# Kernel tuning notes

Hardware: AMD Instinct MI355X
Metric: run time of the kernel (lower is better)

## Reference

```python
import jax, jax.numpy as jnp
import numpy as np

PARTITIONS = [1, 2, 4, 8, 16, 32]
FORECAST = 720
D_MODEL = 256
B, C = 64, 64


def len_of_split_into_k_parts(L, k):
    avg, rem = L // k, L % k
    return [avg + (1 if i < rem else 0) for i in range(k)]


def setup_inputs() -> dict:
    key = jax.random.key(0)
    keys = jax.random.split(key, 1 + 2 * len(PARTITIONS))
    T = sum(PARTITIONS)
    inp = {"x": jax.random.normal(keys[0], (B, C, T, D_MODEL), dtype=jnp.float32)}
    for i, k in enumerate(PARTITIONS):
        max_len = max(len_of_split_into_k_parts(FORECAST, k))
        bound = 1.0 / np.sqrt(D_MODEL)
        inp[f"W{i}"] = jax.random.uniform(keys[1 + 2 * i], (max_len, D_MODEL), minval=-bound, maxval=bound, dtype=jnp.float32)
        inp[f"b{i}"] = jax.random.uniform(keys[2 + 2 * i], (max_len,), minval=-bound, maxval=bound, dtype=jnp.float32)
    return inp


def _forward(x, Ws, bs):
    idx = 0
    total = None
    for i, k in enumerate(PARTITIONS):
        split = len_of_split_into_k_parts(FORECAST, k)
        x_r = x[..., idx:idx + k, :]                      # [B, C, k, d]
        idx += k
        proj = jnp.einsum('bctd,md->bctm', x_r, Ws[i]) + bs[i]  # [B, C, k, max_len]
        # ragged slice+concat: token s contributes its first split[s] positions
        tok = np.repeat(np.arange(k), split)              # [f] static indices
        pos = np.concatenate([np.arange(s) for s in split])  # [f]
        res = proj[..., tok, pos]                         # [B, C, f]
        total = res if total is None else total + res
    return jnp.swapaxes(total, -1, -2)                    # [B, f, C]


def reference(x, W0, b0, W1, b1, W2, b2, W3, b3, W4, b4, W5, b5):
    Ws = [W0, W1, W2, W3, W4, W5]
    bs = [b0, b1, b2, b3, b4, b5]
    return _forward(x, Ws, bs)
```

## Files before the change

kernel.cpp:

```cpp
#include <hip/hip_runtime.h>
#include <stdint.h>


#define FDIM 720
#define DDIM 256
#define TDIM 63
#define NSUBTOT 299
#define TAB_BYTES ((size_t)NSUBTOT * 8 * 1024)
#define OUTELEMS ((size_t)64 * FDIM * 64)
#define NPREPTHR (NSUBTOT * 8 * 64)

typedef __attribute__((ext_vector_type(8))) short short8;
typedef __attribute__((ext_vector_type(4))) float f32x4;

__device__ __forceinline__ uint32_t pkru(float a, float b) {
    uint32_t ua = __builtin_bit_cast(uint32_t, a) + 0x8000u;
    uint32_t ub = __builtin_bit_cast(uint32_t, b) + 0x8000u;
    return __builtin_amdgcn_perm(ub, ua, 0x07060302u);
}
__device__ __forceinline__ short8 loadpack(const float* p) {
    float4 v0 = *(const float4*)p;
    float4 v1 = *(const float4*)(p + 4);
    uint4 u;
    u.x = pkru(v0.x, v0.y);
    u.y = pkru(v0.z, v0.w);
    u.z = pkru(v1.x, v1.y);
    u.w = pkru(v1.z, v1.w);
    return __builtin_bit_cast(short8, u);
}

__device__ __forceinline__ void atomAddF(float* p, float v) {
    unsafeAtomicAdd(p, v);
}

__device__ __forceinline__ void jpos(int i, int f, int& j, int& pos) {
    switch (i) {
        case 0: j = 0;       pos = f;            break;
        case 1: j = f / 360; pos = f - 360 * j;  break;
        case 2: j = f / 180; pos = f - 180 * j;  break;
        case 3: j = f / 90;  pos = f - 90 * j;   break;
        case 4: j = f / 45;  pos = f - 45 * j;   break;
        default:
            if (f < 368) { j = f / 23;  pos = f - 23 * j; }
            else { int g = f - 368; int q = g / 22; j = 16 + q; pos = g - 22 * q; }
            break;
    }
}

__device__ __forceinline__ void tok_params(int tok, int& len, int& ns,
                                           int& start, int& tabsub) {
    if (tok < 1)       { len = 720; ns = 45; start = 0;
                         tabsub = 0; }
    else if (tok < 3)  { int j = tok - 1;  len = 360; ns = 23; start = 360 * j;
                         tabsub = 45 + j * 23; }
    else if (tok < 7)  { int j = tok - 3;  len = 180; ns = 12; start = 180 * j;
                         tabsub = 91 + j * 12; }
    else if (tok < 15) { int j = tok - 7;  len = 90;  ns = 6;  start = 90 * j;
                         tabsub = 139 + j * 6; }
    else if (tok < 31) { int j = tok - 15; len = 45;  ns = 3;  start = 45 * j;
                         tabsub = 187 + j * 3; }
    else               { int j = tok - 31;
                         len = (j < 16) ? 23 : 22;
                         start = (j < 16) ? 23 * j : 368 + 22 * (j - 16);
                         ns = 2; tabsub = 235 + j * 2; }
}

__global__ __launch_bounds__(256) void olrs_prepinit(
    const float* __restrict__ W0, const float* __restrict__ W1,
    const float* __restrict__ W2, const float* __restrict__ W3,
    const float* __restrict__ W4, const float* __restrict__ W5,
    const float* __restrict__ b0, const float* __restrict__ b1,
    const float* __restrict__ b2, const float* __restrict__ b3,
    const float* __restrict__ b4, const float* __restrict__ b5,
    char* __restrict__ ws, float* __restrict__ out)
{
    const int gid = blockIdx.x * 256 + threadIdx.x;

    const size_t base = (size_t)gid * 4;
    if (base < OUTELEMS) {
        const int f = (int)((base >> 6) % FDIM);
        int j, p;
        float s = b0[f];
        jpos(1, f, j, p); s += b1[p];
        jpos(2, f, j, p); s += b2[p];
        jpos(3, f, j, p); s += b3[p];
        jpos(4, f, j, p); s += b4[p];
        jpos(5, f, j, p); s += b5[p];
        float4 o = {s, s, s, s};
        *(float4*)(out + base) = o;
    }

    if (gid < NPREPTHR) {
        const int lane = gid & 63;
        const int fid  = gid >> 6;
        const int ks = fid & 7;
        const int g  = fid >> 3;

        int len; const float* W; int s;
        if (g < 45)       { W = W0; len = 720; s = g; }
        else if (g < 91)  { int g2 = g - 45;  W = W1; len = 360; s = g2 % 23; }
        else if (g < 139) { int g2 = g - 91;  W = W2; len = 180; s = g2 % 12; }
        else if (g < 187) { int g2 = g - 139; W = W3; len = 90;  s = g2 % 6; }
        else if (g < 235) { int g2 = g - 187; W = W4; len = 45;  s = g2 % 3; }
        else              { int g2 = g - 235; W = W5; int j = g2 >> 1;
                            len = (j < 16) ? 23 : 22; s = g2 & 1; }

        const int m15  = lane & 15;
        const int koct = lane >> 4;
        const int pos  = s * 16 + m15;
        uint4 u = {0u, 0u, 0u, 0u};
        if (pos < len) {
            const float* src = W + (size_t)pos * DDIM + ks * 32 + koct * 8;
            float4 v0 = *(const float4*)src;
            float4 v1 = *(const float4*)(src + 4);
            u.x = pkru(v0.x, v0.y);
            u.y = pkru(v0.z, v0.w);
            u.z = pkru(v1.x, v1.y);
            u.w = pkru(v1.z, v1.w);
        }
        *(uint4*)(ws + (size_t)fid * 1024 + lane * 16) = u;
    }
}

__global__ __launch_bounds__(256) void olrs_main8(
    const float* __restrict__ x,
    const char* __restrict__ ws,
    float* __restrict__ out)
{
    __shared__ char lds[32768];

    const int bid   = blockIdx.x;
    const int rid   = bid >> 7;
    const int ntile = bid & 127;
    const int w     = threadIdx.x >> 6;
    const int lane  = threadIdx.x & 63;
    const int b     = ntile >> 1;
    const int c0    = (ntile & 1) << 5;
    const int m15   = lane & 15;
    const int koct  = lane >> 4;

    int tok, s0, slab;
    bool shx;
    if (rid < 2)      { tok = 0;            s0 = rid * 24 + w * 6; shx = true;  slab = 0; }
    else if (rid < 4) { tok = rid - 1;      s0 = w * 6;            shx = true;  slab = 0; }
    else if (rid < 6) { int tb = 3 + (rid - 4) * 2;
                        tok = tb + (w >> 1); s0 = (w & 1) * 6;     shx = true;  slab = w >> 1; }
    else              { tok = 7 + (rid - 6) * 4 + w; s0 = 0;       shx = false; slab = 0; }

    int len, ns, start, tabsub;
    tok_params(tok, len, ns, start, tabsub);
    const int send = (s0 + 6 < ns) ? (s0 + 6) : ns;

    short8 xl[8], xh[8];
    if (shx) {
        const int nslab   = (rid >= 4 && rid < 6) ? 2 : 1;
        const int tokbase = (rid < 2) ? 0 : ((rid < 4) ? (rid - 1) : 3 + (rid - 4) * 2);
        const int cc = threadIdx.x >> 3;
        const int t8 = threadIdx.x & 7;
        for (int sl = 0; sl < nslab; sl++) {
            const float* src = x + (((size_t)(b * 64 + c0 + cc)) * TDIM + tokbase + sl) * DDIM;
            char* dst = lds + sl * 16384;
            #pragma unroll
            for (int rep = 0; rep < 4; rep++) {
                const int d8 = t8 + rep * 8;
                float4 v0 = *(const float4*)(src + d8 * 8);
                float4 v1 = *(const float4*)(src + d8 * 8 + 4);
                uint4 u;
                u.x = pkru(v0.x, v0.y);
                u.y = pkru(v0.z, v0.w);
                u.z = pkru(v1.x, v1.y);
                u.w = pkru(v1.z, v1.w);
                const int slot = ((d8 >> 2) * 2 + (cc >> 4)) * 64
                               + (d8 & 3) * 16 + (cc & 15);
                *(uint4*)(dst + slot * 16) = u;
            }
        }
        __syncthreads();
        const char* sb = lds + slab * 16384;
        #pragma unroll
        for (int ks = 0; ks < 8; ks++) {
            xl[ks] = *(const short8*)(sb + ((ks * 2 + 0) * 64 + lane) * 16);
            xh[ks] = *(const short8*)(sb + ((ks * 2 + 1) * 64 + lane) * 16);
        }
    } else {
        const float* xpl = x + (((size_t)(b * 64 + c0 + m15)) * TDIM + tok) * DDIM;
        const float* xph = xpl + (size_t)16 * TDIM * DDIM;
        #pragma unroll
        for (int ks = 0; ks < 8; ks++)
            xl[ks] = loadpack(xpl + ks * 32 + koct * 8);
        #pragma unroll
        for (int ks = 0; ks < 8; ks++)
            xh[ks] = loadpack(xph + ks * 32 + koct * 8);
    }

    const char* tab = ws + (size_t)tabsub * 8192 + lane * 16;
    float* obl = out + ((size_t)b * FDIM + start) * 64 + c0 + m15;
    float* obh = obl + 16;

    short8 wA[8], wB[8];

    auto loadW = [&](short8* wreg, int s) {
        const char* t = tab + (size_t)s * 8192;
        #pragma unroll
        for (int ks = 0; ks < 8; ks++)
            wreg[ks] = *(const short8*)(t + ks * 1024);
    };
    auto compute = [&](const short8* wreg, int s) {
        f32x4 al0 = {0.f, 0.f, 0.f, 0.f}, al1 = {0.f, 0.f, 0.f, 0.f};
        f32x4 ah0 = {0.f, 0.f, 0.f, 0.f}, ah1 = {0.f, 0.f, 0.f, 0.f};
        __builtin_amdgcn_s_setprio(1);
        #pragma unroll
        for (int ks = 0; ks < 8; ks += 2) {
            al0 = __builtin_amdgcn_mfma_f32_16x16x32_bf16(wreg[ks],     xl[ks],     al0, 0, 0, 0);
            ah0 = __builtin_amdgcn_mfma_f32_16x16x32_bf16(wreg[ks],     xh[ks],     ah0, 0, 0, 0);
            al1 = __builtin_amdgcn_mfma_f32_16x16x32_bf16(wreg[ks + 1], xl[ks + 1], al1, 0, 0, 0);
            ah1 = __builtin_amdgcn_mfma_f32_16x16x32_bf16(wreg[ks + 1], xh[ks + 1], ah1, 0, 0, 0);
        }
        __builtin_amdgcn_s_setprio(0);
        const int fl0 = s * 16 + koct * 4;
        #pragma unroll
        for (int rg = 0; rg < 4; rg++) {
            const int fl = fl0 + rg;
            if (fl < len) {
                atomAddF(obl + (size_t)fl * 64, al0[rg] + al1[rg]);
                atomAddF(obh + (size_t)fl * 64, ah0[rg] + ah1[rg]);
            }
        }
    };

    int s = s0;
    loadW(wA, s);
    for (;;) {
        if (s + 1 < send) loadW(wB, s + 1);
        compute(wA, s);
        if (++s >= send) break;
        if (s + 1 < send) loadW(wA, s + 1);
        compute(wB, s);
        if (++s >= send) break;
    }
}

__device__ __forceinline__ int startf(int i, int j) {
    switch (i) {
        case 0: return 0;
        case 1: return 360 * j;
        case 2: return 180 * j;
        case 3: return 90 * j;
        case 4: return 45 * j;
        default: return (j < 16) ? 23 * j : 368 + 22 * (j - 16);
    }
}

__global__ __launch_bounds__(256) void olrs_fb(
    const float* __restrict__ x,
    const float* __restrict__ W0, const float* __restrict__ b0,
    const float* __restrict__ W1, const float* __restrict__ b1,
    const float* __restrict__ W2, const float* __restrict__ b2,
    const float* __restrict__ W3, const float* __restrict__ b3,
    const float* __restrict__ W4, const float* __restrict__ b4,
    const float* __restrict__ W5, const float* __restrict__ b5,
    float* __restrict__ out)
{
    const float* Wp[6] = {W0, W1, W2, W3, W4, W5};
    const float* bp[6] = {b0, b1, b2, b3, b4, b5};
    const int TB[6] = {0, 1, 3, 7, 15, 31};

    const int wid  = blockIdx.x * 4 + (threadIdx.x >> 6);
    const int lane = threadIdx.x & 63;
    const int ft   = wid % 45;
    const int bc   = wid / 45;
    const int b    = bc >> 2;
    const int c0   = (bc & 3) << 4;
    const int f0   = ft << 4;
    const int m15  = lane & 15;
    const int koct = lane >> 4;
    const size_t xrow = (size_t)(b * 64 + c0 + m15) * TDIM;

    f32x4 acc = {0.f, 0.f, 0.f, 0.f};
    #pragma unroll
    for (int i = 0; i < 6; i++) {
        int jlo, plo, jhi, phi;
        jpos(i, f0, jlo, plo);
        jpos(i, f0 + 15, jhi, phi);
        const bool cross = (jhi > jlo);
        const int fb = cross ? (startf(i, jhi) - f0) : 16;
        const float* xlo = x + (xrow + TB[i] + jlo) * DDIM;
        const float* xhi = x + (xrow + TB[i] + jhi) * DDIM;
        int jw, pw;
        jpos(i, f0 + m15, jw, pw);
        const float* wsrc = Wp[i] + (size_t)pw * DDIM;
        #pragma unroll
        for (int ks = 0; ks < 8; ks++) {
            const int d0 = ks * 32 + koct * 8;
            short8 a = loadpack(wsrc + d0);
            short8 blo = loadpack(xlo + d0);
            if (!cross) {
                acc = __builtin_amdgcn_mfma_f32_16x16x32_bf16(a, blo, acc, 0, 0, 0);
            } else {
                short8 bhi = loadpack(xhi + d0);
                short8 z;
                #pragma unroll
                for (int q = 0; q < 8; q++) z[q] = 0;
                short8 alo = (m15 < fb) ? a : z;
                short8 ahi = (m15 < fb) ? z : a;
                acc = __builtin_amdgcn_mfma_f32_16x16x32_bf16(alo, blo, acc, 0, 0, 0);
                acc = __builtin_amdgcn_mfma_f32_16x16x32_bf16(ahi, bhi, acc, 0, 0, 0);
            }
        }
    }
    #pragma unroll
    for (int rg = 0; rg < 4; rg++) {
        const int f = f0 + koct * 4 + rg;
        float bias = 0.f;
        #pragma unroll
        for (int i = 0; i < 6; i++) {
            int j, pos;
            jpos(i, f, j, pos);
            bias += bp[i][pos];
        }
        out[((size_t)b * FDIM + f) * 64 + c0 + m15] = acc[rg] + bias;
    }
}

extern "C" void kernel_launch(void* const* d_in, const int* in_sizes, int n_in,
                              void* d_out, int out_size, void* d_ws, size_t ws_size,
                              hipStream_t stream) {
    (void)in_sizes; (void)n_in; (void)out_size;

    const float* x  = (const float*)d_in[0];
    const float* W0 = (const float*)d_in[1];
    const float* b0 = (const float*)d_in[2];
    const float* W1 = (const float*)d_in[3];
    const float* b1 = (const float*)d_in[4];
    const float* W2 = (const float*)d_in[5];
    const float* b2 = (const float*)d_in[6];
    const float* W3 = (const float*)d_in[7];
    const float* b3 = (const float*)d_in[8];
    const float* W4 = (const float*)d_in[9];
    const float* b4 = (const float*)d_in[10];
    const float* W5 = (const float*)d_in[11];
    const float* b5 = (const float*)d_in[12];
    float* out = (float*)d_out;

    if (ws_size >= TAB_BYTES) {
        char* ws = (char*)d_ws;
        olrs_prepinit<<<dim3((unsigned)(OUTELEMS / 4 / 256)), dim3(256), 0, stream>>>(
            W0, W1, W2, W3, W4, W5, b0, b1, b2, b3, b4, b5, ws, out);
        olrs_main8<<<dim3(20 * 128), dim3(256), 0, stream>>>(x, ws, out);
    } else {
        olrs_fb<<<dim3(45 * 256), dim3(256), 0, stream>>>(
            x, W0, b0, W1, b1, W2, b2, W3, b3, W4, b4, W5, b5, out);
    }
}
```

Measured before the change: 86.60 us.

## Halve channel tile per block and drop weight double-buffering

Each block now covers 16 channels instead of 32, which doubles the grid to 5120 blocks and halves both the LDS footprint and the per-thread x registers. The explicit register double-buffering of weight tiles is removed, so weights are loaded inline right before each MFMA pair. The aim is lower register and LDS pressure, giving higher occupancy and more parallelism. The cost is that each weight tile is now fetched twice as often across blocks (once per 16-channel tile), and load latency is no longer hidden by the manual prefetch.

New measurement: 101.7 us. +17.4%, slower.

```diff
diff --git a/kernel.cpp b/kernel.cpp
--- a/kernel.cpp
+++ b/kernel.cpp
@@ -28,7 +28,6 @@
     u.w = pkru(v1.z, v1.w);
     return __builtin_bit_cast(short8, u);
 }
-
 __device__ __forceinline__ void atomAddF(float* p, float v) {
     unsafeAtomicAdd(p, v);
 }
@@ -122,47 +121,47 @@
     }
 }
 
-__global__ __launch_bounds__(256) void olrs_main8(
+__global__ __launch_bounds__(256) void olrs_main13(
     const float* __restrict__ x,
     const char* __restrict__ ws,
     float* __restrict__ out)
 {
-    __shared__ char lds[32768];
+    __shared__ char lds[16384];
 
     const int bid   = blockIdx.x;
-    const int rid   = bid >> 7;
-    const int ntile = bid & 127;
+    const int rid   = bid >> 8;
+    const int ntile = bid & 255;
     const int w     = threadIdx.x >> 6;
     const int lane  = threadIdx.x & 63;
-    const int b     = ntile >> 1;
-    const int c0    = (ntile & 1) << 5;
+    const int b     = ntile >> 2;
+    const int c0    = (ntile & 3) << 4;
     const int m15   = lane & 15;
     const int koct  = lane >> 4;
 
     int tok, s0, slab;
     bool shx;
-    if (rid < 2)      { tok = 0;            s0 = rid * 24 + w * 6; shx = true;  slab = 0; }
-    else if (rid < 4) { tok = rid - 1;      s0 = w * 6;            shx = true;  slab = 0; }
+    if (rid < 2)      { tok = 0;             s0 = rid * 24 + w * 6; shx = true;  slab = 0; }
+    else if (rid < 4) { tok = rid - 1;       s0 = w * 6;            shx = true;  slab = 0; }
     else if (rid < 6) { int tb = 3 + (rid - 4) * 2;
-                        tok = tb + (w >> 1); s0 = (w & 1) * 6;     shx = true;  slab = w >> 1; }
-    else              { tok = 7 + (rid - 6) * 4 + w; s0 = 0;       shx = false; slab = 0; }
+                        tok = tb + (w >> 1); s0 = (w & 1) * 6;      shx = true;  slab = w >> 1; }
+    else              { tok = 7 + (rid - 6) * 4 + w; s0 = 0;        shx = false; slab = 0; }
 
     int len, ns, start, tabsub;
     tok_params(tok, len, ns, start, tabsub);
     const int send = (s0 + 6 < ns) ? (s0 + 6) : ns;
 
-    short8 xl[8], xh[8];
+    short8 xf[8];
     if (shx) {
         const int nslab   = (rid >= 4 && rid < 6) ? 2 : 1;
         const int tokbase = (rid < 2) ? 0 : ((rid < 4) ? (rid - 1) : 3 + (rid - 4) * 2);
-        const int cc = threadIdx.x >> 3;
-        const int t8 = threadIdx.x & 7;
+        const int cc  = threadIdx.x >> 4;
+        const int t16 = threadIdx.x & 15;
         for (int sl = 0; sl < nslab; sl++) {
             const float* src = x + (((size_t)(b * 64 + c0 + cc)) * TDIM + tokbase + sl) * DDIM;
-            char* dst = lds + sl * 16384;
+            char* dst = lds + sl * 8192;
             #pragma unroll
-            for (int rep = 0; rep < 4; rep++) {
-                const int d8 = t8 + rep * 8;
+            for (int rep = 0; rep < 2; rep++) {
+                const int d8 = t16 + rep * 16;
                 float4 v0 = *(const float4*)(src + d8 * 8);
                 float4 v1 = *(const float4*)(src + d8 * 8 + 4);
                 uint4 u;
@@ -170,73 +169,44 @@
                 u.y = pkru(v0.z, v0.w);
                 u.z = pkru(v1.x, v1.y);
                 u.w = pkru(v1.z, v1.w);
-                const int slot = ((d8 >> 2) * 2 + (cc >> 4)) * 64
-                               + (d8 & 3) * 16 + (cc & 15);
+                const int slot = (d8 >> 2) * 64 + (d8 & 3) * 16 + cc;
                 *(uint4*)(dst + slot * 16) = u;
             }
         }
         __syncthreads();
-        const char* sb = lds + slab * 16384;
-        #pragma unroll
-        for (int ks = 0; ks < 8; ks++) {
-            xl[ks] = *(const short8*)(sb + ((ks * 2 + 0) * 64 + lane) * 16);
-            xh[ks] = *(const short8*)(sb + ((ks * 2 + 1) * 64 + lane) * 16);
-        }
+        const char* sb = lds + slab * 8192;
+        #pragma unroll
+        for (int ks = 0; ks < 8; ks++)
+            xf[ks] = *(const short8*)(sb + (ks * 64 + lane) * 16);
     } else {
-        const float* xpl = x + (((size_t)(b * 64 + c0 + m15)) * TDIM + tok) * DDIM;
-        const float* xph = xpl + (size_t)16 * TDIM * DDIM;
+        const float* xp = x + (((size_t)(b * 64 + c0 + m15)) * TDIM + tok) * DDIM;
         #pragma unroll
         for (int ks = 0; ks < 8; ks++)
-            xl[ks] = loadpack(xpl + ks * 32 + koct * 8);
-        #pragma unroll
-        for (int ks = 0; ks < 8; ks++)
-            xh[ks] = loadpack(xph + ks * 32 + koct * 8);
+            xf[ks] = loadpack(xp + ks * 32 + koct * 8);
     }
 
     const char* tab = ws + (size_t)tabsub * 8192 + lane * 16;
-    float* obl = out + ((size_t)b * FDIM + start) * 64 + c0 + m15;
-    float* obh = obl + 16;
-
-    short8 wA[8], wB[8];
-
-    auto loadW = [&](short8* wreg, int s) {
-        const char* t = tab + (size_t)s * 8192;
-        #pragma unroll
-        for (int ks = 0; ks < 8; ks++)
-            wreg[ks] = *(const short8*)(t + ks * 1024);
-    };
-    auto compute = [&](const short8* wreg, int s) {
-        f32x4 al0 = {0.f, 0.f, 0.f, 0.f}, al1 = {0.f, 0.f, 0.f, 0.f};
-        f32x4 ah0 = {0.f, 0.f, 0.f, 0.f}, ah1 = {0.f, 0.f, 0.f, 0.f};
+    float* obase = out + ((size_t)b * FDIM + start) * 64 + c0 + m15;
+
+    for (int s = s0; s < send; s++) {
+        f32x4 a0 = {0.f, 0.f, 0.f, 0.f};
+        f32x4 a1 = {0.f, 0.f, 0.f, 0.f};
+        const char* tsub = tab + (size_t)s * 8192;
         __builtin_amdgcn_s_setprio(1);
         #pragma unroll
         for (int ks = 0; ks < 8; ks += 2) {
-            al0 = __builtin_amdgcn_mfma_f32_16x16x32_bf16(wreg[ks],     xl[ks],     al0, 0, 0, 0);
-            ah0 = __builtin_amdgcn_mfma_f32_16x16x32_bf16(wreg[ks],     xh[ks],     ah0, 0, 0, 0);
-            al1 = __builtin_amdgcn_mfma_f32_16x16x32_bf16(wreg[ks + 1], xl[ks + 1], al1, 0, 0, 0);
-            ah1 = __builtin_amdgcn_mfma_f32_16x16x32_bf16(wreg[ks + 1], xh[ks + 1], ah1, 0, 0, 0);
+            short8 w0 = *(const short8*)(tsub + ks * 1024);
+            short8 w1 = *(const short8*)(tsub + (ks + 1) * 1024);
+            a0 = __builtin_amdgcn_mfma_f32_16x16x32_bf16(w0, xf[ks],     a0, 0, 0, 0);
+            a1 = __builtin_amdgcn_mfma_f32_16x16x32_bf16(w1, xf[ks + 1], a1, 0, 0, 0);
         }
         __builtin_amdgcn_s_setprio(0);
         const int fl0 = s * 16 + koct * 4;
         #pragma unroll
         for (int rg = 0; rg < 4; rg++) {
             const int fl = fl0 + rg;
-            if (fl < len) {
-                atomAddF(obl + (size_t)fl * 64, al0[rg] + al1[rg]);
-                atomAddF(obh + (size_t)fl * 64, ah0[rg] + ah1[rg]);
-            }
-        }
-    };
-
-    int s = s0;
-    loadW(wA, s);
-    for (;;) {
-        if (s + 1 < send) loadW(wB, s + 1);
-        compute(wA, s);
-        if (++s >= send) break;
-        if (s + 1 < send) loadW(wA, s + 1);
-        compute(wB, s);
-        if (++s >= send) break;
+            if (fl < len) atomAddF(obase + (size_t)fl * 64, a0[rg] + a1[rg]);
+        }
     }
 }
 
@@ -346,7 +316,7 @@
         char* ws = (char*)d_ws;
         olrs_prepinit<<<dim3((unsigned)(OUTELEMS / 4 / 256)), dim3(256), 0, stream>>>(
             W0, W1, W2, W3, W4, W5, b0, b1, b2, b3, b4, b5, ws, out);
-        olrs_main8<<<dim3(20 * 128), dim3(256), 0, stream>>>(x, ws, out);
+        olrs_main13<<<dim3(20 * 256), dim3(256), 0, stream>>>(x, ws, out);
     } else {
         olrs_fb<<<dim3(45 * 256), dim3(256), 0, stream>>>(
             x, W0, b0, W1, b1, W2, b2, W3, b3, W4, b4, W5, b5, out);
```

## Share weight tiles via LDS across waves for small-token partitions

Applied to the files above, without the earlier changes.

Blocks for the later partitions (tokens 7 and up) are remapped: each block now stages that token's bf16 weight sub-tiles into LDS once, and its four waves each handle a different (batch, channel) tile while reading weights from shared memory. Previously every wave fetched its own weights from global memory. The token-8 group is also split into two halves of three sub-tiles for more parallelism. The grid grows from 2560 to 2816 blocks and adds a barrier plus LDS staging per block, in exchange for less redundant global weight traffic.

New measurement: 92.44 us. 6.7% more time.

```diff
diff --git a/kernel.cpp b/kernel.cpp
--- a/kernel.cpp
+++ b/kernel.cpp
@@ -122,7 +122,7 @@
     }
 }
 
-__global__ __launch_bounds__(256) void olrs_main8(
+__global__ __launch_bounds__(256) void olrs_main15(
     const float* __restrict__ x,
     const char* __restrict__ ws,
     float* __restrict__ out)
@@ -130,30 +130,28 @@
     __shared__ char lds[32768];
 
     const int bid   = blockIdx.x;
-    const int rid   = bid >> 7;
-    const int ntile = bid & 127;
     const int w     = threadIdx.x >> 6;
     const int lane  = threadIdx.x & 63;
-    const int b     = ntile >> 1;
-    const int c0    = (ntile & 1) << 5;
     const int m15   = lane & 15;
     const int koct  = lane >> 4;
 
-    int tok, s0, slab;
-    bool shx;
-    if (rid < 2)      { tok = 0;            s0 = rid * 24 + w * 6; shx = true;  slab = 0; }
-    else if (rid < 4) { tok = rid - 1;      s0 = w * 6;            shx = true;  slab = 0; }
-    else if (rid < 6) { int tb = 3 + (rid - 4) * 2;
-                        tok = tb + (w >> 1); s0 = (w & 1) * 6;     shx = true;  slab = w >> 1; }
-    else              { tok = 7 + (rid - 6) * 4 + w; s0 = 0;       shx = false; slab = 0; }
-
-    int len, ns, start, tabsub;
-    tok_params(tok, len, ns, start, tabsub);
-    const int send = (s0 + 6 < ns) ? (s0 + 6) : ns;
-
-    short8 xl[8], xh[8];
-    if (shx) {
-        const int nslab   = (rid >= 4 && rid < 6) ? 2 : 1;
+    if (bid < 768) {
+        const int rid   = bid >> 7;
+        const int ntile = bid & 127;
+        const int b     = ntile >> 1;
+        const int c0    = (ntile & 1) << 5;
+
+        int tok, s0, slab;
+        if (rid < 2)      { tok = 0;             s0 = rid * 24 + w * 6; slab = 0; }
+        else if (rid < 4) { tok = rid - 1;       s0 = w * 6;            slab = 0; }
+        else              { int tb = 3 + (rid - 4) * 2;
+                            tok = tb + (w >> 1); s0 = (w & 1) * 6;      slab = w >> 1; }
+
+        int len, ns, start, tabsub;
+        tok_params(tok, len, ns, start, tabsub);
+        const int send = (s0 + 6 < ns) ? (s0 + 6) : ns;
+
+        const int nslab   = (rid >= 4) ? 2 : 1;
         const int tokbase = (rid < 2) ? 0 : ((rid < 4) ? (rid - 1) : 3 + (rid - 4) * 2);
         const int cc = threadIdx.x >> 3;
         const int t8 = threadIdx.x & 7;
@@ -176,67 +174,126 @@
             }
         }
         __syncthreads();
+        short8 xl[8], xh[8];
         const char* sb = lds + slab * 16384;
         #pragma unroll
         for (int ks = 0; ks < 8; ks++) {
             xl[ks] = *(const short8*)(sb + ((ks * 2 + 0) * 64 + lane) * 16);
             xh[ks] = *(const short8*)(sb + ((ks * 2 + 1) * 64 + lane) * 16);
         }
+
+        const char* tab = ws + (size_t)tabsub * 8192 + lane * 16;
+        float* obl = out + ((size_t)b * FDIM + start) * 64 + c0 + m15;
+        float* obh = obl + 16;
+
+        short8 wA[8], wB[8];
+        auto loadW = [&](short8* wreg, int s) {
+            const char* t = tab + (size_t)s * 8192;
+            #pragma unroll
+            for (int ks = 0; ks < 8; ks++)
+                wreg[ks] = *(const short8*)(t + ks * 1024);
+        };
+        auto compute = [&](const short8* wreg, int s) {
+            f32x4 al0 = {0.f, 0.f, 0.f, 0.f}, al1 = {0.f, 0.f, 0.f, 0.f};
+            f32x4 ah0 = {0.f, 0.f, 0.f, 0.f}, ah1 = {0.f, 0.f, 0.f, 0.f};
+            __builtin_amdgcn_s_setprio(1);
+            #pragma unroll
+            for (int ks = 0; ks < 8; ks += 2) {
+                al0 = __builtin_amdgcn_mfma_f32_16x16x32_bf16(wreg[ks],     xl[ks],     al0, 0, 0, 0);
+                ah0 = __builtin_amdgcn_mfma_f32_16x16x32_bf16(wreg[ks],     xh[ks],     ah0, 0, 0, 0);
+                al1 = __builtin_amdgcn_mfma_f32_16x16x32_bf16(wreg[ks + 1], xl[ks + 1], al1, 0, 0, 0);
+                ah1 = __builtin_amdgcn_mfma_f32_16x16x32_bf16(wreg[ks + 1], xh[ks + 1], ah1, 0, 0, 0);
+            }
+            __builtin_amdgcn_s_setprio(0);
+            const int fl0 = s * 16 + koct * 4;
+            #pragma unroll
+            for (int rg = 0; rg < 4; rg++) {
+                const int fl = fl0 + rg;
+                if (fl < len) {
+                    atomAddF(obl + (size_t)fl * 64, al0[rg] + al1[rg]);
+                    atomAddF(obh + (size_t)fl * 64, ah0[rg] + ah1[rg]);
+                }
+            }
+        };
+
+        int s = s0;
+        loadW(wA, s);
+        for (;;) {
+            if (s + 1 < send) loadW(wB, s + 1);
+            compute(wA, s);
+            if (++s >= send) break;
+            if (s + 1 < send) loadW(wA, s + 1);
+            compute(wB, s);
+            if (++s >= send) break;
+        }
     } else {
+        const int idx = bid - 768;
+        int tok, s0g, g;
+        if (idx < 512)       { int q = idx >> 5; g = idx & 31;
+                               tok = 7 + (q >> 1); s0g = (q & 1) * 3; }
+        else if (idx < 1024) { int q = idx - 512; g = q & 31;
+                               tok = 15 + (q >> 5); s0g = 0; }
+        else                 { int q = idx - 1024; g = q & 31;
+                               tok = 31 + (q >> 5); s0g = 0; }
+
+        int len, ns, start, tabsub;
+        tok_params(tok, len, ns, start, tabsub);
+        const int send = (s0g + 3 < ns) ? (s0g + 3) : ns;
+        const int nsub = send - s0g;
+
+        const int ntile = g * 4 + w;
+        const int b     = ntile >> 1;
+        const int c0    = (ntile & 1) << 5;
+
+        {
+            const char* src = ws + (size_t)(tabsub + s0g) * 8192;
+            const int nrep = nsub * 2;
+            for (int r = 0; r < nrep; r++) {
+                const int off = threadIdx.x * 16 + r * 4096;
+                *(uint4*)(lds + off) = *(const uint4*)(src + off);
+            }
+        }
+
         const float* xpl = x + (((size_t)(b * 64 + c0 + m15)) * TDIM + tok) * DDIM;
         const float* xph = xpl + (size_t)16 * TDIM * DDIM;
+        short8 xl[8], xh[8];
         #pragma unroll
         for (int ks = 0; ks < 8; ks++)
             xl[ks] = loadpack(xpl + ks * 32 + koct * 8);
         #pragma unroll
         for (int ks = 0; ks < 8; ks++)
             xh[ks] = loadpack(xph + ks * 32 + koct * 8);
-    }
-
-    const char* tab = ws + (size_t)tabsub * 8192 + lane * 16;
-    float* obl = out + ((size_t)b * FDIM + start) * 64 + c0 + m15;
-    float* obh = obl + 16;
-
-    short8 wA[8], wB[8];
-
-    auto loadW = [&](short8* wreg, int s) {
-        const char* t = tab + (size_t)s * 8192;
-        #pragma unroll
-        for (int ks = 0; ks < 8; ks++)
-            wreg[ks] = *(const short8*)(t + ks * 1024);
-    };
-    auto compute = [&](const short8* wreg, int s) {
-        f32x4 al0 = {0.f, 0.f, 0.f, 0.f}, al1 = {0.f, 0.f, 0.f, 0.f};
-        f32x4 ah0 = {0.f, 0.f, 0.f, 0.f}, ah1 = {0.f, 0.f, 0.f, 0.f};
-        __builtin_amdgcn_s_setprio(1);
-        #pragma unroll
-        for (int ks = 0; ks < 8; ks += 2) {
-            al0 = __builtin_amdgcn_mfma_f32_16x16x32_bf16(wreg[ks],     xl[ks],     al0, 0, 0, 0);
-            ah0 = __builtin_amdgcn_mfma_f32_16x16x32_bf16(wreg[ks],     xh[ks],     ah0, 0, 0, 0);
-            al1 = __builtin_amdgcn_mfma_f32_16x16x32_bf16(wreg[ks + 1], xl[ks + 1], al1, 0, 0, 0);
-            ah1 = __builtin_amdgcn_mfma_f32_16x16x32_bf16(wreg[ks + 1], xh[ks + 1], ah1, 0, 0, 0);
-        }
-        __builtin_amdgcn_s_setprio(0);
-        const int fl0 = s * 16 + koct * 4;
-        #pragma unroll
-        for (int rg = 0; rg < 4; rg++) {
-            const int fl = fl0 + rg;
-            if (fl < len) {
-                atomAddF(obl + (size_t)fl * 64, al0[rg] + al1[rg]);
-                atomAddF(obh + (size_t)fl * 64, ah0[rg] + ah1[rg]);
-            }
-        }
-    };
-
-    int s = s0;
-    loadW(wA, s);
-    for (;;) {
-        if (s + 1 < send) loadW(wB, s + 1);
-        compute(wA, s);
-        if (++s >= send) break;
-        if (s + 1 < send) loadW(wA, s + 1);
-        compute(wB, s);
-        if (++s >= send) break;
+
+        __syncthreads();
+
+        float* obl = out + ((size_t)b * FDIM + start) * 64 + c0 + m15;
+        float* obh = obl + 16;
+
+        for (int s = s0g; s < send; s++) {
+            const char* tsub = lds + (size_t)(s - s0g) * 8192 + lane * 16;
+            f32x4 al0 = {0.f, 0.f, 0.f, 0.f}, al1 = {0.f, 0.f, 0.f, 0.f};
+            f32x4 ah0 = {0.f, 0.f, 0.f, 0.f}, ah1 = {0.f, 0.f, 0.f, 0.f};
+            __builtin_amdgcn_s_setprio(1);
+            #pragma unroll
+            for (int ks = 0; ks < 8; ks += 2) {
+                short8 w0 = *(const short8*)(tsub + ks * 1024);
+                short8 w1 = *(const short8*)(tsub + (ks + 1) * 1024);
+                al0 = __builtin_amdgcn_mfma_f32_16x16x32_bf16(w0, xl[ks],     al0, 0, 0, 0);
+                ah0 = __builtin_amdgcn_mfma_f32_16x16x32_bf16(w0, xh[ks],     ah0, 0, 0, 0);
+                al1 = __builtin_amdgcn_mfma_f32_16x16x32_bf16(w1, xl[ks + 1], al1, 0, 0, 0);
+                ah1 = __builtin_amdgcn_mfma_f32_16x16x32_bf16(w1, xh[ks + 1], ah1, 0, 0, 0);
+            }
+            __builtin_amdgcn_s_setprio(0);
+            const int fl0 = s * 16 + koct * 4;
+            #pragma unroll
+            for (int rg = 0; rg < 4; rg++) {
+                const int fl = fl0 + rg;
+                if (fl < len) {
+                    atomAddF(obl + (size_t)fl * 64, al0[rg] + al1[rg]);
+                    atomAddF(obh + (size_t)fl * 64, ah0[rg] + ah1[rg]);
+                }
+            }
+        }
     }
 }
 
@@ -346,7 +403,7 @@
         char* ws = (char*)d_ws;
         olrs_prepinit<<<dim3((unsigned)(OUTELEMS / 4 / 256)), dim3(256), 0, stream>>>(
             W0, W1, W2, W3, W4, W5, b0, b1, b2, b3, b4, b5, ws, out);
-        olrs_main8<<<dim3(20 * 128), dim3(256), 0, stream>>>(x, ws, out);
+        olrs_main15<<<dim3(2816), dim3(256), 0, stream>>>(x, ws, out);
     } else {
         olrs_fb<<<dim3(45 * 256), dim3(256), 0, stream>>>(
             x, W0, b0, W1, b1, W2, b2, W3, b3, W4, b4, W5, b5, out);
```
